# Kernel tuning notes

Measured on AMD Instinct MI355X. Metric: run time of the kernel, lower is better.

Reference implementation:

```python
import jax, jax.numpy as jnp
import numpy as np
import math

B, S, HID = 1, 2048, 4096
HQ, HKV, D = 32, 8, 128
G = HQ // HKV          # GQA group size
OBS, W, SINK = 128, 32, 2
THETA = 500000.0
TOP_FRAC, MID_SPARSITY, LOW_FRAC = 0.05, 0.7, 0.20
K_KEEP = int(math.ceil((1.0 - MID_SPARSITY) * D))  # elements kept per level-1 token


def _rope(x):
    # x: [B, H, S, D]; standard Llama rotary embedding
    half = D // 2
    inv_freq = 1.0 / (THETA ** (jnp.arange(half, dtype=jnp.float32) / half))
    ang = jnp.arange(S, dtype=jnp.float32)[:, None] * inv_freq[None, :]  # [S, half]
    cos = jnp.concatenate([jnp.cos(ang), jnp.cos(ang)], axis=-1)  # [S, D]
    sin = jnp.concatenate([jnp.sin(ang), jnp.sin(ang)], axis=-1)
    x1, x2 = x[..., :half], x[..., half:]
    rot = jnp.concatenate([-x2, x1], axis=-1)
    return x * cos[None, None] + rot * sin[None, None]


def _topk_mask(x):
    # keep the K_KEEP largest-magnitude elements of each length-D token vector
    a = jnp.abs(x)
    thr = jnp.sort(a, axis=-1)[..., D - K_KEEP]
    return a >= thr[..., None]


def setup_inputs() -> dict:
    key = jax.random.key(0)
    ks = jax.random.split(key, 5)
    sc = HID ** -0.5
    return {
        "hidden_states": jax.random.normal(ks[0], (B, S, HID), dtype=jnp.float32),
        "wq": jax.random.normal(ks[1], (HID, HQ * D), dtype=jnp.float32) * sc,
        "wk": jax.random.normal(ks[2], (HID, HKV * D), dtype=jnp.float32) * sc,
        "wv": jax.random.normal(ks[3], (HID, HKV * D), dtype=jnp.float32) * sc,
        "wo": jax.random.normal(ks[4], (HQ * D, HID), dtype=jnp.float32) * sc,
    }


def reference(hidden_states, wq, wk, wv, wo):
    scale = 1.0 / math.sqrt(D)
    q = (hidden_states @ wq).reshape(B, S, HQ, D).transpose(0, 2, 1, 3)   # [B,HQ,S,D]
    k = (hidden_states @ wk).reshape(B, S, HKV, D).transpose(0, 2, 1, 3)  # [B,HKV,S,D]
    v = (hidden_states @ wv).reshape(B, S, HKV, D).transpose(0, 2, 1, 3)
    q, k = _rope(q), _rope(k)

    # --- observation-window GQA attention (grouped queries vs all keys) ---
    obs_q = q[:, :, S - OBS:, :].reshape(B, HKV, G, OBS, D)
    s_obs = jnp.einsum('bhgqd,bhkd->bhgqk', obs_q, k) * scale
    obs_causal = jnp.arange(S)[None, :] <= (S - OBS + jnp.arange(OBS))[:, None]  # [OBS,S]
    s_obs = jnp.where(obs_causal[None, None, None], s_obs, -jnp.inf)
    aw_kv = jax.nn.softmax(s_obs.astype(jnp.float32), axis=-1).mean(axis=2)  # [B,HKV,OBS,S]

    # per-token importance, normalized by how many obs queries observed each key
    counts = jnp.minimum(OBS, S - jnp.arange(S)).astype(jnp.float32)
    imp = aw_kv.sum(axis=2) / counts[None, None, :]  # [B,HKV,S]

    # --- global thresholds over the compressible region -> 3 sparsity levels ---
    imp_c = imp[:, :, :S - W].reshape(-1)
    t_high = jnp.quantile(imp_c, 1.0 - TOP_FRAC)
    t_low = jnp.quantile(imp_c, LOW_FRAC)
    level = jnp.where(imp >= t_high, 0, jnp.where(imp < t_low, 2, 1))
    pos = jnp.arange(S)
    dense_pos = (pos >= S - W) | (pos < SINK)     # recent window + sinks stay dense
    level = jnp.where(dense_pos[None, None, :], 0, level)

    keep_k = jnp.where((level == 0)[..., None], True, (level == 1)[..., None] & _topk_mask(k))
    keep_v = jnp.where((level == 0)[..., None], True, (level == 1)[..., None] & _topk_mask(v))
    k_sp = k * keep_k
    v_sp = v * keep_v
    evicted = level == 2

    # --- causal GQA attention over the sparsified KV cache ---
    q_g = q.reshape(B, HKV, G, S, D)
    s = jnp.einsum('bhgqd,bhkd->bhgqk', q_g, k_sp) * scale
    causal = jnp.tril(jnp.ones((S, S), dtype=bool))
    allow = causal[None, None, None] & (~evicted)[:, :, None, None, :]
    s = jnp.where(allow, s, -jnp.inf)
    p = jax.nn.softmax(s.astype(jnp.float32), axis=-1).astype(v_sp.dtype)
    o = jnp.einsum('bhgqk,bhkd->bhgqd', p, v_sp)
    o = o.reshape(B, HQ, S, D).transpose(0, 2, 1, 3).reshape(B, S, HQ * D)
    return o @ wo
```

## Files before the change

### kernel.cpp

```cpp
#include <hip/hip_runtime.h>
#include <hip/hip_bf16.h>
#include <math.h>

#define S_    2048
#define HID_  4096
#define HQ_   32
#define HKV_  8
#define D_    128
#define G_    4
#define OBS_  128
#define W_    32
#define NKV_  1024
#define NQ_   4096
#define KLD_  2048
#define SCALE_ 0.08838834764831845f
#define THR_IDX_ 89
#define NC_   16128

typedef __attribute__((ext_vector_type(4))) float f32x4;
typedef __attribute__((ext_vector_type(8))) short s16x8;
typedef __attribute__((ext_vector_type(8))) unsigned short u16x8;
typedef __attribute__((ext_vector_type(4))) unsigned short u16x4;
typedef unsigned short ushort_t;

struct TermPtrs { const ushort_t* a[6]; const ushort_t* b[6]; };

__device__ __forceinline__ unsigned short f2bf(float x) {
  union { float f; unsigned u; } v; v.f = x;
  unsigned r = v.u + 0x7FFFu + ((v.u >> 16) & 1u);
  return (unsigned short)(r >> 16);
}
__device__ __forceinline__ float bf2f(unsigned short b) {
  union { unsigned u; float f; } v; v.u = ((unsigned)b) << 16;
  return v.f;
}
__device__ __forceinline__ void gload_lds16(const void* g, void* l) {
  __builtin_amdgcn_global_load_lds((const __attribute__((address_space(1))) unsigned int*)g,
                                   (__attribute__((address_space(3))) unsigned int*)l, 16, 0, 0);
}
__device__ __forceinline__ void term_sel(const TermPtrs& P, int tt,
                                         const ushort_t*& As, const ushort_t*& Bs) {
  switch (tt) {
    case 0: As = P.a[0]; Bs = P.b[0]; break;
    case 1: As = P.a[1]; Bs = P.b[1]; break;
    case 2: As = P.a[2]; Bs = P.b[2]; break;
    case 3: As = P.a[3]; Bs = P.b[3]; break;
    case 4: As = P.a[4]; Bs = P.b[4]; break;
    default: As = P.a[5]; Bs = P.b[5]; break;
  }
}

__global__ __launch_bounds__(256) void split3_kernel(const float* __restrict__ src,
                                                     ushort_t* __restrict__ d0,
                                                     ushort_t* __restrict__ d1,
                                                     ushort_t* __restrict__ d2, int n4) {
  int idx = blockIdx.x * 256 + threadIdx.x;
  if (idx >= n4) return;
  float4 v = ((const float4*)src)[idx];
  u16x4 o0, o1, o2;
  float xs[4] = {v.x, v.y, v.z, v.w};
#pragma unroll
  for (int e = 0; e < 4; ++e) {
    float x = xs[e];
    unsigned short b0 = f2bf(x);
    float r = x - bf2f(b0);
    unsigned short b1 = f2bf(r);
    float r2 = r - bf2f(b1);
    o0[e] = b0; o1[e] = b1; o2[e] = f2bf(r2);
  }
  *(u16x4*)(d0 + (size_t)idx * 4) = o0;
  *(u16x4*)(d1 + (size_t)idx * 4) = o1;
  *(u16x4*)(d2 + (size_t)idx * 4) = o2;
}

__global__ __launch_bounds__(256) void splitT_kernel(const float* __restrict__ src, int N,
                                                     ushort_t* __restrict__ t0,
                                                     ushort_t* __restrict__ t1,
                                                     ushort_t* __restrict__ t2) {
  __shared__ float tile[64][65];
  const int t = threadIdx.x;
  const int n0 = blockIdx.x * 64, k0 = blockIdx.y * 64;
#pragma unroll
  for (int i = 0; i < 16; ++i) {
    int idx = i * 256 + t;
    int r = idx >> 6, c = idx & 63;
    tile[r][c] = src[(size_t)(k0 + r) * N + n0 + c];
  }
  __syncthreads();
#pragma unroll
  for (int i = 0; i < 16; ++i) {
    int idx = i * 256 + t;
    int n = idx >> 6, kk = idx & 63;
    float x = tile[kk][n];
    unsigned short b0 = f2bf(x);
    size_t o = (size_t)(n0 + n) * HID_ + k0 + kk;
    t0[o] = b0;
    if (t1) {
      float r = x - bf2f(b0);
      unsigned short b1 = f2bf(r);
      t1[o] = b1;
      t2[o] = f2bf(r - bf2f(b1));
    }
  }
}

template<int TPZ>
__global__ __launch_bounds__(256) void gemm6(TermPtrs P, float* __restrict__ Cbase,
                                             int M, int N, int K) {
  __shared__ ushort_t lds[2 * 128 * 64];
  const int t = threadIdx.x;
  const int wave = t >> 6, lane = t & 63;
  const int lc = lane & 15, lg = lane >> 4;
  const int bm = blockIdx.y, bn = blockIdx.x, z = blockIdx.z;
  const int wm = wave >> 1, wn = wave & 1;
  const int srow = t >> 3, schunk = t & 7;
  float* C = Cbase + (size_t)z * M * N;

  f32x4 acc[4][4];
#pragma unroll
  for (int fi = 0; fi < 4; ++fi)
#pragma unroll
    for (int fj = 0; fj < 4; ++fj) acc[fi][fj] = 0.f;

  for (int tt = z * TPZ; tt < z * TPZ + TPZ; ++tt) {
    const ushort_t *As, *Bs;
    term_sel(P, tt, As, Bs);
    for (int kb = 0; kb < K / 64; ++kb) {
      __syncthreads();
#pragma unroll
      for (int g = 0; g < 4; ++g) {
        int row = g * 32 + srow;
        int sw = schunk ^ (row & 7);
        gload_lds16(As + (size_t)(bm * 128 + row) * K + kb * 64 + sw * 8,
                    lds + g * 2048 + wave * 512);
        gload_lds16(Bs + (size_t)(bn * 128 + row) * K + kb * 64 + sw * 8,
                    lds + 8192 + g * 2048 + wave * 512);
      }
      __syncthreads();
#pragma unroll
      for (int ks = 0; ks < 2; ++ks) {
        s16x8 af[4], bf[4];
#pragma unroll
        for (int f = 0; f < 4; ++f) {
          int ra = wm * 64 + f * 16 + lc;
          af[f] = *(const s16x8*)(lds + ra * 64 + (((ks * 4 + lg) ^ (ra & 7)) * 8));
          int rb = wn * 64 + f * 16 + lc;
          bf[f] = *(const s16x8*)(lds + 8192 + rb * 64 + (((ks * 4 + lg) ^ (rb & 7)) * 8));
        }
#pragma unroll
        for (int fi = 0; fi < 4; ++fi)
#pragma unroll
          for (int fj = 0; fj < 4; ++fj)
            acc[fi][fj] = __builtin_amdgcn_mfma_f32_16x16x32_bf16(af[fi], bf[fj], acc[fi][fj], 0, 0, 0);
      }
    }
  }
#pragma unroll
  for (int fi = 0; fi < 4; ++fi)
#pragma unroll
    for (int fj = 0; fj < 4; ++fj)
#pragma unroll
      for (int r = 0; r < 4; ++r)
        C[(size_t)(bm * 128 + wm * 64 + fi * 16 + lg * 4 + r) * N +
          bn * 128 + wn * 64 + fj * 16 + lc] = acc[fi][fj][r];
}

__global__ __launch_bounds__(256) void gemm6k(TermPtrs P, float* __restrict__ Cp, int N) {
  __shared__ ushort_t lds[2 * 128 * 64];
  const int t = threadIdx.x;
  const int wave = t >> 6, lane = t & 63;
  const int lc = lane & 15, lg = lane >> 4;
  const int bn = blockIdx.x, z = blockIdx.z;
  const int wm = wave >> 1, wn = wave & 1;
  const int srow = t >> 3, schunk = t & 7;
  float* C = Cp + (size_t)z * 128 * N;

  f32x4 acc[4][4];
#pragma unroll
  for (int fi = 0; fi < 4; ++fi)
#pragma unroll
    for (int fj = 0; fj < 4; ++fj) acc[fi][fj] = 0.f;

  for (int tt = 0; tt < 6; ++tt) {
    const ushort_t *As, *Bs;
    term_sel(P, tt, As, Bs);
    for (int kb = z * 8; kb < z * 8 + 8; ++kb) {
      __syncthreads();
#pragma unroll
      for (int g = 0; g < 4; ++g) {
        int row = g * 32 + srow;
        int sw = schunk ^ (row & 7);
        gload_lds16(As + (size_t)row * HID_ + kb * 64 + sw * 8,
                    lds + g * 2048 + wave * 512);
        gload_lds16(Bs + (size_t)(bn * 128 + row) * HID_ + kb * 64 + sw * 8,
                    lds + 8192 + g * 2048 + wave * 512);
      }
      __syncthreads();
#pragma unroll
      for (int ks = 0; ks < 2; ++ks) {
        s16x8 af[4], bf[4];
#pragma unroll
        for (int f = 0; f < 4; ++f) {
          int ra = wm * 64 + f * 16 + lc;
          af[f] = *(const s16x8*)(lds + ra * 64 + (((ks * 4 + lg) ^ (ra & 7)) * 8));
          int rb = wn * 64 + f * 16 + lc;
          bf[f] = *(const s16x8*)(lds + 8192 + rb * 64 + (((ks * 4 + lg) ^ (rb & 7)) * 8));
        }
#pragma unroll
        for (int fi = 0; fi < 4; ++fi)
#pragma unroll
          for (int fj = 0; fj < 4; ++fj)
            acc[fi][fj] = __builtin_amdgcn_mfma_f32_16x16x32_bf16(af[fi], bf[fj], acc[fi][fj], 0, 0, 0);
      }
    }
  }
#pragma unroll
  for (int fi = 0; fi < 4; ++fi)
#pragma unroll
    for (int fj = 0; fj < 4; ++fj)
#pragma unroll
      for (int r = 0; r < 4; ++r)
        C[(size_t)(wm * 64 + fi * 16 + lg * 4 + r) * N +
          bn * 128 + wn * 64 + fj * 16 + lc] = acc[fi][fj][r];
}

__global__ __launch_bounds__(256) void gemm6z(TermPtrs P, float* __restrict__ Cg) {
  __shared__ ushort_t lds[2 * 128 * 64];
  const int t = threadIdx.x;
  const int wave = t >> 6, lane = t & 63;
  const int lc = lane & 15, lg = lane >> 4;
  const int bm = blockIdx.y, bn = blockIdx.x, z = blockIdx.z;
  const int wm = wave >> 1, wn = wave & 1;
  const int srow = t >> 3, schunk = t & 7;
  const size_t Aoff = (size_t)z * 512 * 128;
  const size_t Boff = (size_t)z * 2048 * 128;
  float* C = Cg + (size_t)z * 512 * 2048;

  f32x4 acc[4][4];
#pragma unroll
  for (int fi = 0; fi < 4; ++fi)
#pragma unroll
    for (int fj = 0; fj < 4; ++fj) acc[fi][fj] = 0.f;

  for (int tt = 0; tt < 6; ++tt) {
    const ushort_t *As, *Bs;
    term_sel(P, tt, As, Bs);
    As += Aoff; Bs += Boff;
    for (int kb = 0; kb < 2; ++kb) {
      __syncthreads();
#pragma unroll
      for (int g = 0; g < 4; ++g) {
        int row = g * 32 + srow;
        int sw = schunk ^ (row & 7);
        gload_lds16(As + (size_t)(bm * 128 + row) * 128 + kb * 64 + sw * 8,
                    lds + g * 2048 + wave * 512);
        gload_lds16(Bs + (size_t)(bn * 128 + row) * 128 + kb * 64 + sw * 8,
                    lds + 8192 + g * 2048 + wave * 512);
      }
      __syncthreads();
#pragma unroll
      for (int ks = 0; ks < 2; ++ks) {
        s16x8 af[4], bf[4];
#pragma unroll
        for (int f = 0; f < 4; ++f) {
          int ra = wm * 64 + f * 16 + lc;
          af[f] = *(const s16x8*)(lds + ra * 64 + (((ks * 4 + lg) ^ (ra & 7)) * 8));
          int rb = wn * 64 + f * 16 + lc;
          bf[f] = *(const s16x8*)(lds + 8192 + rb * 64 + (((ks * 4 + lg) ^ (rb & 7)) * 8));
        }
#pragma unroll
        for (int fi = 0; fi < 4; ++fi)
#pragma unroll
          for (int fj = 0; fj < 4; ++fj)
            acc[fi][fj] = __builtin_amdgcn_mfma_f32_16x16x32_bf16(af[fi], bf[fj], acc[fi][fj], 0, 0, 0);
      }
    }
  }
#pragma unroll
  for (int fi = 0; fi < 4; ++fi)
#pragma unroll
    for (int fj = 0; fj < 4; ++fj)
#pragma unroll
      for (int r = 0; r < 4; ++r)
        C[(size_t)(bm * 128 + wm * 64 + fi * 16 + lg * 4 + r) * 2048 +
          bn * 128 + wn * 64 + fj * 16 + lc] = acc[fi][fj][r];
}

__global__ void reduce3_kernel(const float* __restrict__ p, float* __restrict__ out, int n4) {
  int idx = blockIdx.x * 256 + threadIdx.x;
  if (idx >= n4) return;
  const size_t n = (size_t)n4 * 4;
  float4 a = ((const float4*)p)[idx];
  float4 b = ((const float4*)(p + n))[idx];
  float4 c = ((const float4*)(p + 2 * n))[idx];
  float4 o;
  o.x = a.x + b.x + c.x; o.y = a.y + b.y + c.y;
  o.z = a.z + b.z + c.z; o.w = a.w + b.w + c.w;
  ((float4*)out)[idx] = o;
}
__global__ void reduce8_kernel(const float* __restrict__ Cp, float* __restrict__ out, int n) {
  int idx = blockIdx.x * 256 + threadIdx.x;
  if (idx >= n) return;
  float s = 0.f;
#pragma unroll
  for (int z = 0; z < 8; ++z) s += Cp[(size_t)z * n + idx];
  out[idx] = s;
}

__global__ void freq_kernel(float* __restrict__ invf) {
  int j = threadIdx.x;
  if (j < 64) invf[j] = (float)(1.0 / pow(500000.0, (double)j / 64.0));
}

__global__ void rope_kernel(float* __restrict__ X, ushort_t* __restrict__ Xb,
                            const float* __restrict__ invf, int H, int ld, int pos0, int total) {
  int idx = blockIdx.x * 256 + threadIdx.x;
  if (idx >= total) return;
  int j = idx & 63;
  int h = (idx >> 6) % H;
  int s = idx / (64 * H);
  float ang = (float)(pos0 + s) * invf[j];
  float sn, cs;
  sincosf(ang, &sn, &cs);
  size_t base = (size_t)s * ld + h * D_ + j;
  float x1 = X[base], x2 = X[base + 64];
  float o1 = x1 * cs - x2 * sn;
  float o2 = x2 * cs + x1 * sn;
  X[base] = o1; X[base + 64] = o2;
  if (Xb) { Xb[base] = f2bf(o1); Xb[base + 64] = f2bf(o2); }
}

__global__ __launch_bounds__(256) void splitq_obs(const float* __restrict__ qobs,
                                                  ushort_t* __restrict__ q0,
                                                  ushort_t* __restrict__ q1,
                                                  ushort_t* __restrict__ q2) {
  int idx = blockIdx.x * 256 + threadIdx.x;
  if (idx >= OBS_ * NQ_ / 4) return;
  int idx4 = idx * 4;
  int i = idx4 >> 12;
  int col = idx4 & 4095;
  int hq = col >> 7, d = col & 127;
  int hk = hq >> 2, g = hq & 3;
  float4 v = *(const float4*)(qobs + (size_t)i * NQ_ + col);
  size_t o = (size_t)hk * 65536 + (size_t)(g * 128 + i) * 128 + d;
  float xs[4] = {v.x, v.y, v.z, v.w};
  u16x4 o0, o1, o2;
#pragma unroll
  for (int e = 0; e < 4; ++e) {
    float x = xs[e];
    unsigned short b0 = f2bf(x);
    float r = x - bf2f(b0);
    unsigned short b1 = f2bf(r);
    o0[e] = b0; o1[e] = b1; o2[e] = f2bf(r - bf2f(b1));
  }
  *(u16x4*)(q0 + o) = o0;
  *(u16x4*)(q1 + o) = o1;
  *(u16x4*)(q2 + o) = o2;
}

__global__ __launch_bounds__(256) void splitk_obs(const float* __restrict__ kvf,
                                                  ushort_t* __restrict__ k0,
                                                  ushort_t* __restrict__ k1,
                                                  ushort_t* __restrict__ k2) {
  int idx = blockIdx.x * 256 + threadIdx.x;
  if (idx >= S_ * NKV_ / 4) return;
  int idx4 = idx * 4;
  int j = idx4 >> 10;
  int col = idx4 & 1023;
  int hk = col >> 7, d = col & 127;
  float4 v = *(const float4*)(kvf + (size_t)j * KLD_ + col);
  size_t o = (size_t)hk * 262144 + ((size_t)j << 7) + d;
  float xs[4] = {v.x, v.y, v.z, v.w};
  u16x4 o0, o1, o2;
#pragma unroll
  for (int e = 0; e < 4; ++e) {
    float x = xs[e];
    unsigned short b0 = f2bf(x);
    float r = x - bf2f(b0);
    unsigned short b1 = f2bf(r);
    o0[e] = b0; o1[e] = b1; o2[e] = f2bf(r - bf2f(b1));
  }
  *(u16x4*)(k0 + o) = o0;
  *(u16x4*)(k1 + o) = o1;
  *(u16x4*)(k2 + o) = o2;
}

__global__ __launch_bounds__(256) void rowstat_kernel(const float* __restrict__ s,
                                                      float* __restrict__ mx,
                                                      float* __restrict__ dinv) {
  const int row = blockIdx.x * 4 + (threadIdx.x >> 6);
  const int lane = threadIdx.x & 63;
  const int i = row & 127;
  const int jmax = S_ - OBS_ + i;
  const float* sp = s + (size_t)row * S_;
  float vals[32];
  float m = -INFINITY;
#pragma unroll
  for (int c = 0; c < 8; ++c) {
    int j0 = c * 256 + lane * 4;
    float4 v = *(const float4*)(sp + j0);
    float e0 = (j0 + 0 <= jmax) ? v.x * SCALE_ : -INFINITY;
    float e1 = (j0 + 1 <= jmax) ? v.y * SCALE_ : -INFINITY;
    float e2 = (j0 + 2 <= jmax) ? v.z * SCALE_ : -INFINITY;
    float e3 = (j0 + 3 <= jmax) ? v.w * SCALE_ : -INFINITY;
    vals[c * 4 + 0] = e0; vals[c * 4 + 1] = e1; vals[c * 4 + 2] = e2; vals[c * 4 + 3] = e3;
    m = fmaxf(m, fmaxf(fmaxf(e0, e1), fmaxf(e2, e3)));
  }
#pragma unroll
  for (int off = 1; off < 64; off <<= 1) m = fmaxf(m, __shfl_xor(m, off, 64));
  float ssum = 0.f;
#pragma unroll
  for (int c = 0; c < 32; ++c) ssum += expf(vals[c] - m);
#pragma unroll
  for (int off = 1; off < 64; off <<= 1) ssum += __shfl_xor(ssum, off, 64);
  if (lane == 0) { mx[row] = m; dinv[row] = 1.0f / ssum; }
}

__global__ __launch_bounds__(256) void colsum_part(const float* __restrict__ s,
                                                   const float* __restrict__ mx,
                                                   const float* __restrict__ dinv,
                                                   float* __restrict__ part) {
  __shared__ float mxl[64], dvl[64];
  const int jt = blockIdx.x, hk = blockIdx.y, rc = blockIdx.z;
  const int t = threadIdx.x;
  if (t < 64) {
    mxl[t] = mx[hk * 512 + rc * 64 + t];
    dvl[t] = dinv[hk * 512 + rc * 64 + t];
  }
  __syncthreads();
  const int j = jt * 256 + t;
  const float* sp = s + ((size_t)hk * 512 + rc * 64) * S_ + j;
  float acc = 0.f;
  for (int rr = 0; rr < 64; ++rr) {
    int i = (rc * 64 + rr) & 127;
    if (j <= S_ - OBS_ + i)
      acc += expf(sp[(size_t)rr * S_] * SCALE_ - mxl[rr]) * dvl[rr];
  }
  part[((size_t)rc * 8 + hk) * S_ + j] = acc;
}

__global__ void colsum_fin(const float* __restrict__ part, float* __restrict__ imp) {
  int idx = blockIdx.x * 256 + threadIdx.x;
  int hk = idx >> 11, j = idx & 2047;
  float acc = 0.f;
#pragma unroll
  for (int rc = 0; rc < 8; ++rc) acc += part[((size_t)rc * 8 + hk) * S_ + j];
  float cnt = (float)min(OBS_, S_ - j);
  imp[idx] = acc * 0.25f / cnt;
}

__global__ __launch_bounds__(1024) void radix_all(const float* __restrict__ imp,
                                                  float* __restrict__ thr) {
  __shared__ unsigned hist[4][256];
  __shared__ unsigned pfx_s[4], need_s[4];
  const int t = threadIdx.x;
  if (t < 4) {
    pfx_s[t] = 0u;
    need_s[t] = (t == 0) ? 3225u : (t == 1) ? 3226u : (t == 2) ? 15320u : 15321u;
  }
  __syncthreads();
  for (int pass = 0; pass < 4; ++pass) {
    ((unsigned*)hist)[t] = 0u;
    __syncthreads();
    int shift = 24 - pass * 8;
    for (int idx = t; idx < NC_; idx += 1024) {
      int h = idx / (S_ - W_), j = idx - h * (S_ - W_);
      union { float f; unsigned u; } cv; cv.f = imp[h * S_ + j];
      unsigned u = cv.u;
#pragma unroll
      for (int q = 0; q < 4; ++q) {
        bool m = (pass == 0) || ((u >> (shift + 8)) == (pfx_s[q] >> (shift + 8)));
        if (m) atomicAdd(&hist[q][(u >> shift) & 255u], 1u);
      }
    }
    __syncthreads();
    if (t < 4) {
      unsigned need = need_s[t], cum = 0, pfx = pfx_s[t];
      for (int d = 0; d < 256; ++d) {
        unsigned c = hist[t][d];
        if (cum + c > need) { pfx |= ((unsigned)d) << shift; need_s[t] = need - cum; break; }
        cum += c;
      }
      pfx_s[t] = pfx;
    }
    __syncthreads();
  }
  if (t == 0) {
    union { unsigned u; float f; } c0, c1, c2, c3;
    c0.u = pfx_s[0]; c1.u = pfx_s[1]; c2.u = pfx_s[2]; c3.u = pfx_s[3];
    double fl = 0.2 * (double)(NC_ - 1) - 3225.0;
    double fh = 0.95 * (double)(NC_ - 1) - 15320.0;
    thr[0] = (float)((double)c2.f + ((double)c3.f - (double)c2.f) * fh);
    thr[1] = (float)((double)c0.f + ((double)c1.f - (double)c0.f) * fl);
  }
}

__global__ __launch_bounds__(128) void sparsify_kernel(const float* __restrict__ kv,
                                                       const float* __restrict__ imp,
                                                       const float* __restrict__ thr,
                                                       ushort_t* __restrict__ ksp,
                                                       ushort_t* __restrict__ vsp,
                                                       float* __restrict__ ebias) {
  const int b = blockIdx.x;
  const int j = b >> 3;
  const int h = b & 7;
  const int t = threadIdx.x;
  float ipv = imp[h * S_ + j];
  bool dense = (j >= S_ - W_) || (j < 2);
  int lvl = dense ? 0 : ((ipv >= thr[0]) ? 0 : ((ipv < thr[1]) ? 2 : 1));
  if (t == 0) ebias[h * S_ + j] = (lvl == 2) ? -INFINITY : 0.0f;
  __shared__ float av[128];
  __shared__ float thv;
  size_t base_in = (size_t)j * KLD_ + h * D_;
  size_t base_out = (size_t)j * NKV_ + h * D_;
  float kvv = kv[base_in + t];
  av[t] = fabsf(kvv);
  __syncthreads();
  {
    float at = av[t]; int cnt = 0;
    for (int m = 0; m < 128; ++m) { float am = av[m]; cnt += (am < at) || (am == at && m < t); }
    if (cnt == THR_IDX_) thv = at;
  }
  __syncthreads();
  {
    bool keep = (lvl == 0) || (lvl == 1 && fabsf(kvv) >= thv);
    ksp[base_out + t] = f2bf(keep ? kvv : 0.0f);
  }
  __syncthreads();
  float vvv = kv[base_in + 1024 + t];
  av[t] = fabsf(vvv);
  __syncthreads();
  {
    float at = av[t]; int cnt = 0;
    for (int m = 0; m < 128; ++m) { float am = av[m]; cnt += (am < at) || (am == at && m < t); }
    if (cnt == THR_IDX_) thv = at;
  }
  __syncthreads();
  {
    bool keep = (lvl == 0) || (lvl == 1 && fabsf(vvv) >= thv);
    vsp[base_out + t] = f2bf(keep ? vvv : 0.0f);
  }
}

__global__ __launch_bounds__(256) void vtrans_kernel(const ushort_t* __restrict__ vsp,
                                                     ushort_t* __restrict__ vspT) {
  __shared__ ushort_t tl[64][136];
  const int jt = blockIdx.x;
  const int hk = blockIdx.y;
  const int t = threadIdx.x;
#pragma unroll
  for (int i = 0; i < 4; ++i) {
    int idx = i * 256 + t;
    int j = idx >> 4, c = idx & 15;
    *(u16x8*)&tl[j][c * 8] = *(const u16x8*)(vsp + (size_t)(jt * 64 + j) * NKV_ + hk * 128 + c * 8);
  }
  __syncthreads();
  int d = t >> 1, j0 = (t & 1) * 32;
#pragma unroll
  for (int jj = 0; jj < 4; ++jj) {
    u16x8 v;
#pragma unroll
    for (int e = 0; e < 8; ++e) v[e] = tl[j0 + jj * 8 + e][d];
    *(u16x8*)(vspT + ((size_t)hk * 128 + d) * S_ + jt * 64 + j0 + jj * 8) = v;
  }
}

#define SPAD_ 66
__global__ __launch_bounds__(256) void attn_kernel(const ushort_t* __restrict__ qbp,
                                                   const ushort_t* __restrict__ ksp,
                                                   const ushort_t* __restrict__ vspT,
                                                   const float* __restrict__ ebias,
                                                   ushort_t* __restrict__ ob16) {
  __shared__ ushort_t k_lds[64 * 128];
  __shared__ ushort_t vT_lds[128 * 64];
  __shared__ float s_lds[4][16][SPAD_];
  const int b = blockIdx.x;
  const int xcd = b & 7;
  const int idx = b >> 3;
  const int h = xcd * 4 + (idx >> 4);
  const int p = idx & 15;
  const int hk = h >> 2;
  const int t = threadIdx.x;
  const int w = t >> 6, lane = t & 63;
  const int lc = lane & 15, lg = lane >> 4;

  const ushort_t* kbase = ksp + hk * D_;
  const ushort_t* vbase = vspT + (size_t)hk * D_ * S_;

  for (int strip = 0; strip < 2; ++strip) {
    const int qb = (strip == 0) ? p : 31 - p;
    const int q0 = qb * 64 + w * 16;
    s16x8 qfrag[4];
#pragma unroll
    for (int db = 0; db < 4; ++db)
      qfrag[db] = *(const s16x8*)(qbp + (size_t)(q0 + lc) * NQ_ + h * D_ + db * 32 + lg * 8);

    f32x4 o[8];
#pragma unroll
    for (int n = 0; n < 8; ++n) o[n] = 0.f;
    float mr[4] = {-INFINITY, -INFINITY, -INFINITY, -INFINITY};
    float lr[4] = {0.f, 0.f, 0.f, 0.f};

    const int ntj = qb + 1;
    for (int tj = 0; tj < ntj; ++tj) {
      const int j0 = tj * 64;
      __syncthreads();
#pragma unroll
      for (int i = 0; i < 4; ++i) {
        int slot = i * 256 + w * 64 + lane;
        int row = slot >> 4, c = slot & 15;
        const ushort_t* gp = kbase + (size_t)(j0 + row) * NKV_ + ((c ^ (row & 7)) * 8);
        gload_lds16(gp, &k_lds[(i * 256 + w * 64) * 8]);
      }
#pragma unroll
      for (int i = 0; i < 4; ++i) {
        int slot = i * 256 + w * 64 + lane;
        int d = slot >> 3, c = slot & 7;
        const ushort_t* gp = vbase + (size_t)d * S_ + j0 + ((c ^ (d & 7)) * 8);
        gload_lds16(gp, &vT_lds[(i * 256 + w * 64) * 8]);
      }
      __syncthreads();

      f32x4 sfr[4];
#pragma unroll
      for (int js = 0; js < 4; ++js) sfr[js] = 0.f;
#pragma unroll
      for (int js = 0; js < 4; ++js) {
        int row = js * 16 + lc;
#pragma unroll
        for (int db = 0; db < 4; ++db) {
          s16x8 kf = *(const s16x8*)&k_lds[row * 128 + (((db * 4 + lg) ^ (lc & 7)) * 8)];
          sfr[js] = __builtin_amdgcn_mfma_f32_16x16x32_bf16(qfrag[db], kf, sfr[js], 0, 0, 0);
        }
      }
      float eb[4];
#pragma unroll
      for (int js = 0; js < 4; ++js) eb[js] = ebias[hk * S_ + j0 + js * 16 + lc];

      const bool diag = (tj == qb);
      float sclv[4];
#pragma unroll
      for (int r = 0; r < 4; ++r) {
        float sv[4];
#pragma unroll
        for (int js = 0; js < 4; ++js) sv[js] = sfr[js][r] * SCALE_ + eb[js];
        if (diag) {
          int qrow = w * 16 + lg * 4 + r;
#pragma unroll
          for (int js = 0; js < 4; ++js)
            if (js * 16 + lc > qrow) sv[js] = -INFINITY;
        }
        float tm = fmaxf(fmaxf(sv[0], sv[1]), fmaxf(sv[2], sv[3]));
#pragma unroll
        for (int off = 1; off < 16; off <<= 1) tm = fmaxf(tm, __shfl_xor(tm, off, 64));
        float mnew = fmaxf(mr[r], tm);
        float scl = __expf(mr[r] - mnew);
        float ps = 0.f;
#pragma unroll
        for (int js = 0; js < 4; ++js) {
          float e = __expf(sv[js] - mnew);
          s_lds[w][lg * 4 + r][js * 16 + lc] = e;
          ps += e;
        }
#pragma unroll
        for (int off = 1; off < 16; off <<= 1) ps += __shfl_xor(ps, off, 64);
        lr[r] = lr[r] * scl + ps;
        mr[r] = mnew;
        sclv[r] = scl;
      }
#pragma unroll
      for (int n = 0; n < 8; ++n) {
        f32x4 ov = o[n];
#pragma unroll
        for (int r = 0; r < 4; ++r) ov[r] *= sclv[r];
        o[n] = ov;
      }
      asm volatile("s_waitcnt lgkmcnt(0)" ::: "memory");
      s16x8 pa[2];
#pragma unroll
      for (int ks = 0; ks < 2; ++ks) {
        float pv[8];
        *(f32x4*)&pv[0] = *(const f32x4*)&s_lds[w][lc][ks * 32 + lg * 8];
        *(f32x4*)&pv[4] = *(const f32x4*)&s_lds[w][lc][ks * 32 + lg * 8 + 4];
        s16x8 pk;
#pragma unroll
        for (int e = 0; e < 8; ++e) pk[e] = (short)f2bf(pv[e]);
        pa[ks] = pk;
      }
#pragma unroll
      for (int n = 0; n < 8; ++n) {
        int d = n * 16 + lc;
#pragma unroll
        for (int ks = 0; ks < 2; ++ks) {
          s16x8 vf = *(const s16x8*)&vT_lds[d * 64 + (((ks * 4 + lg) ^ (lc & 7)) * 8)];
          o[n] = __builtin_amdgcn_mfma_f32_16x16x32_bf16(pa[ks], vf, o[n], 0, 0, 0);
        }
      }
    }
#pragma unroll
    for (int r = 0; r < 4; ++r) {
      float rinv = 1.0f / lr[r];
      int row = q0 + lg * 4 + r;
#pragma unroll
      for (int n = 0; n < 8; ++n)
        ob16[(size_t)row * NQ_ + h * D_ + n * 16 + lc] = f2bf(o[n][r] * rinv);
    }
  }
}

extern "C" void kernel_launch(void* const* d_in, const int* in_sizes, int n_in,
                              void* d_out, int out_size, void* d_ws, size_t ws_size,
                              hipStream_t stream) {
  (void)in_sizes; (void)n_in; (void)out_size; (void)ws_size;
  const float* hid = (const float*)d_in[0];
  const float* wq  = (const float*)d_in[1];
  const float* wk  = (const float*)d_in[2];
  const float* wv  = (const float*)d_in[3];
  const float* wo  = (const float*)d_in[4];
  float* out = (float*)d_out;
  char* ws = (char*)d_ws;
  const size_t MB = 1ull << 20;

  ushort_t* h0     = (ushort_t*)(ws + 0 * MB);
  ushort_t* h1     = (ushort_t*)(ws + 16 * MB);
  ushort_t* h2     = (ushort_t*)(ws + 32 * MB);
  ushort_t* wq0T   = (ushort_t*)(ws + 48 * MB);
  ushort_t* wq1T   = (ushort_t*)(ws + 80 * MB);
  ushort_t* wq2T   = (ushort_t*)(ws + 112 * MB);
  ushort_t* wkv0T  = (ushort_t*)(ws + 144 * MB);
  ushort_t* wkv1T  = (ushort_t*)(ws + 160 * MB);
  ushort_t* wkv2T  = (ushort_t*)(ws + 176 * MB);
  float*    qpart  = (float*)(ws + 192 * MB);
  float*    qobs   = (float*)(ws + 208 * MB);
  float*    kvf    = (float*)(ws + 210 * MB);
  float*    kvp    = (float*)(ws + 80 * MB);
  float*    qf     = (float*)(ws + 80 * MB);
  ushort_t* qb16   = (ushort_t*)(ws + 112 * MB);
  float*    s_obs  = (float*)(ws + 0 * MB);
  ushort_t* woT    = (ushort_t*)(ws + 144 * MB);
  ushort_t* ksp    = (ushort_t*)(ws + 176 * MB);
  ushort_t* vsp    = (ushort_t*)(ws + 180 * MB);
  ushort_t* vspT   = (ushort_t*)(ws + 184 * MB);
  ushort_t* ob16   = (ushort_t*)(ws + 188 * MB);
  ushort_t* qo0    = (ushort_t*)(ws + 32 * MB);
  ushort_t* qo1    = (ushort_t*)(ws + 33 * MB);
  ushort_t* qo2    = (ushort_t*)(ws + 34 * MB);
  ushort_t* kb0    = (ushort_t*)(ws + 35 * MB);
  ushort_t* kb1    = (ushort_t*)(ws + 39 * MB);
  ushort_t* kb2    = (ushort_t*)(ws + 43 * MB);
  char*     misc   = ws + 226 * MB;
  float*    impv   = (float*)(misc + 0);
  float*    eb     = (float*)(misc + 64 * 1024);
  float*    invf   = (float*)(misc + 128 * 1024);
  float*    thr    = (float*)(misc + 132 * 1024);
  float*    mxbuf  = (float*)(misc + 160 * 1024);
  float*    dinvb  = (float*)(misc + 192 * 1024);
  float*    part   = (float*)(misc + 256 * 1024);

  split3_kernel<<<(S_ * HID_ / 4 + 255) / 256, 256, 0, stream>>>(hid, h0, h1, h2, S_ * HID_ / 4);
  splitT_kernel<<<dim3(NQ_ / 64, HID_ / 64), 256, 0, stream>>>(wq, NQ_, wq0T, wq1T, wq2T);
  splitT_kernel<<<dim3(NKV_ / 64, HID_ / 64), 256, 0, stream>>>(wk, NKV_, wkv0T, wkv1T, wkv2T);
  splitT_kernel<<<dim3(NKV_ / 64, HID_ / 64), 256, 0, stream>>>(
      wv, NKV_, wkv0T + (size_t)NKV_ * HID_, wkv1T + (size_t)NKV_ * HID_, wkv2T + (size_t)NKV_ * HID_);

  const size_t obs_off = (size_t)(S_ - OBS_) * HID_;
  {
    TermPtrs P;
    P.a[0] = h0 + obs_off; P.b[0] = wq0T;
    P.a[1] = h0 + obs_off; P.b[1] = wq1T;
    P.a[2] = h1 + obs_off; P.b[2] = wq0T;
    P.a[3] = h1 + obs_off; P.b[3] = wq1T;
    P.a[4] = h0 + obs_off; P.b[4] = wq2T;
    P.a[5] = h2 + obs_off; P.b[5] = wq0T;
    gemm6k<<<dim3(NQ_ / 128, 1, 8), 256, 0, stream>>>(P, qpart, NQ_);
  }
  reduce8_kernel<<<(OBS_ * NQ_ + 255) / 256, 256, 0, stream>>>(qpart, qobs, OBS_ * NQ_);

  {
    TermPtrs P;
    P.a[0] = h0; P.b[0] = wkv0T;
    P.a[1] = h0; P.b[1] = wkv1T;
    P.a[2] = h1; P.b[2] = wkv0T;
    P.a[3] = h1; P.b[3] = wkv1T;
    P.a[4] = h0; P.b[4] = wkv2T;
    P.a[5] = h2; P.b[5] = wkv0T;
    gemm6<2><<<dim3(KLD_ / 128, S_ / 128, 3), 256, 0, stream>>>(P, kvp, S_, KLD_, HID_);
  }
  reduce3_kernel<<<(S_ * KLD_ / 4 + 255) / 256, 256, 0, stream>>>(kvp, kvf, S_ * KLD_ / 4);

  {
    TermPtrs P;
    for (int i = 0; i < 6; ++i) { P.a[i] = h0; P.b[i] = wq0T; }
    gemm6<1><<<dim3(NQ_ / 128, S_ / 128, 1), 256, 0, stream>>>(P, qf, S_, NQ_, HID_);
  }

  splitT_kernel<<<dim3(HID_ / 64, HID_ / 64), 256, 0, stream>>>(wo, HID_, woT, nullptr, nullptr);

  freq_kernel<<<1, 64, 0, stream>>>(invf);
  rope_kernel<<<(S_ * HQ_ * 64 + 255) / 256, 256, 0, stream>>>(qf, qb16, invf, HQ_, NQ_, 0, S_ * HQ_ * 64);
  rope_kernel<<<(S_ * HKV_ * 64 + 255) / 256, 256, 0, stream>>>(kvf, nullptr, invf, HKV_, KLD_, 0, S_ * HKV_ * 64);
  rope_kernel<<<(OBS_ * HQ_ * 64 + 255) / 256, 256, 0, stream>>>(qobs, nullptr, invf, HQ_, NQ_, S_ - OBS_, OBS_ * HQ_ * 64);

  splitq_obs<<<(OBS_ * NQ_ / 4 + 255) / 256, 256, 0, stream>>>(qobs, qo0, qo1, qo2);
  splitk_obs<<<(S_ * NKV_ / 4 + 255) / 256, 256, 0, stream>>>(kvf, kb0, kb1, kb2);
  {
    TermPtrs P;
    P.a[0] = qo0; P.b[0] = kb0;
    P.a[1] = qo0; P.b[1] = kb1;
    P.a[2] = qo1; P.b[2] = kb0;
    P.a[3] = qo1; P.b[3] = kb1;
    P.a[4] = qo0; P.b[4] = kb2;
    P.a[5] = qo2; P.b[5] = kb0;
    gemm6z<<<dim3(16, 4, 8), 256, 0, stream>>>(P, s_obs);
  }
  rowstat_kernel<<<1024, 256, 0, stream>>>(s_obs, mxbuf, dinvb);
  colsum_part<<<dim3(8, 8, 8), 256, 0, stream>>>(s_obs, mxbuf, dinvb, part);
  colsum_fin<<<64, 256, 0, stream>>>(part, impv);

  radix_all<<<1, 1024, 0, stream>>>(impv, thr);

  sparsify_kernel<<<S_ * HKV_, 128, 0, stream>>>(kvf, impv, thr, ksp, vsp, eb);
  vtrans_kernel<<<dim3(S_ / 64, HKV_), 256, 0, stream>>>(vsp, vspT);
  attn_kernel<<<512, 256, 0, stream>>>(qb16, ksp, vspT, eb, ob16);
  {
    TermPtrs P;
    for (int i = 0; i < 6; ++i) { P.a[i] = ob16; P.b[i] = woT; }
    gemm6<1><<<dim3(HID_ / 128, S_ / 128, 1), 256, 0, stream>>>(P, out, S_, HID_, HID_);
  }
}
```

Measured before the change: 973.7 us.

## Share operand tiles in KV split GEMM, split-K Q/O GEMMs, fuse RoPE with splits

The KV projection GEMM now loads one shared operand tile plus two partner tiles per z-slice, so each LDS stage feeds two MFMAs and redundant global loads of the shared operand are avoided. The full-Q and output projection GEMMs use a two-way split-K to raise block count, with the partial sums folded into the RoPE kernel or a small reduce. Separate reduce, RoPE and bf16-split kernels for the observation queries and keys are merged into single passes. In exchange, LDS use rises, the split-K path adds extra partial-buffer traffic and a reduction, and the workspace buffer offsets are reshuffled.

```diff
diff --git a/kernel.cpp b/kernel.cpp
--- a/kernel.cpp
+++ b/kernel.cpp
@@ -24,6 +24,7 @@
 typedef unsigned short ushort_t;
 
 struct TermPtrs { const ushort_t* a[6]; const ushort_t* b[6]; };
+struct KvSh { const ushort_t* S[3]; const ushort_t* U0[3]; const ushort_t* U1[3]; int ash[3]; };
 
 __device__ __forceinline__ unsigned short f2bf(float x) {
   union { float f; unsigned u; } v; v.f = x;
@@ -65,8 +66,7 @@
     unsigned short b0 = f2bf(x);
     float r = x - bf2f(b0);
     unsigned short b1 = f2bf(r);
-    float r2 = r - bf2f(b1);
-    o0[e] = b0; o1[e] = b1; o2[e] = f2bf(r2);
+    o0[e] = b0; o1[e] = b1; o2[e] = f2bf(r - bf2f(b1));
   }
   *(u16x4*)(d0 + (size_t)idx * 4) = o0;
   *(u16x4*)(d1 + (size_t)idx * 4) = o1;
@@ -104,9 +104,86 @@
   }
 }
 
-template<int TPZ>
-__global__ __launch_bounds__(256) void gemm6(TermPtrs P, float* __restrict__ Cbase,
-                                             int M, int N, int K) {
+__global__ __launch_bounds__(256) void gemm_kvsh(KvSh P, float* __restrict__ Cbase,
+                                                 int M, int N, int K) {
+  __shared__ ushort_t lds[3 * 128 * 64];
+  const int t = threadIdx.x;
+  const int wave = t >> 6, lane = t & 63;
+  const int lc = lane & 15, lg = lane >> 4;
+  const int bm = blockIdx.y, bn = blockIdx.x, z = blockIdx.z;
+  const int wm = wave >> 1, wn = wave & 1;
+  const int srow = t >> 3, schunk = t & 7;
+  const int ash = P.ash[z];
+  const ushort_t* Sp  = P.S[z];
+  const ushort_t* U0p = P.U0[z];
+  const ushort_t* U1p = P.U1[z];
+  float* C = Cbase + (size_t)z * M * N;
+  const int sbase = (ash ? bm : bn) * 128;
+  const int ubase = (ash ? bn : bm) * 128;
+
+  f32x4 acc[4][4];
+#pragma unroll
+  for (int fi = 0; fi < 4; ++fi)
+#pragma unroll
+    for (int fj = 0; fj < 4; ++fj) acc[fi][fj] = 0.f;
+
+  for (int kb = 0; kb < K / 64; ++kb) {
+    __syncthreads();
+#pragma unroll
+    for (int g = 0; g < 4; ++g) {
+      int row = g * 32 + srow;
+      int sw = schunk ^ (row & 7);
+      size_t co = kb * 64 + sw * 8;
+      gload_lds16(Sp  + (size_t)(sbase + row) * K + co, lds + g * 2048 + wave * 512);
+      gload_lds16(U0p + (size_t)(ubase + row) * K + co, lds + 8192 + g * 2048 + wave * 512);
+      gload_lds16(U1p + (size_t)(ubase + row) * K + co, lds + 16384 + g * 2048 + wave * 512);
+    }
+    __syncthreads();
+#pragma unroll
+    for (int ks = 0; ks < 2; ++ks) {
+      s16x8 sf[4], u0f[4], u1f[4];
+#pragma unroll
+      for (int f = 0; f < 4; ++f) {
+        int rs = (ash ? wm : wn) * 64 + f * 16 + lc;
+        sf[f] = *(const s16x8*)(lds + rs * 64 + (((ks * 4 + lg) ^ (rs & 7)) * 8));
+        int ru = (ash ? wn : wm) * 64 + f * 16 + lc;
+        int cu = (((ks * 4 + lg) ^ (ru & 7)) * 8);
+        u0f[f] = *(const s16x8*)(lds + 8192 + ru * 64 + cu);
+        u1f[f] = *(const s16x8*)(lds + 16384 + ru * 64 + cu);
+      }
+      if (ash) {
+#pragma unroll
+        for (int fi = 0; fi < 4; ++fi)
+#pragma unroll
+          for (int fj = 0; fj < 4; ++fj) {
+            acc[fi][fj] = __builtin_amdgcn_mfma_f32_16x16x32_bf16(sf[fi], u0f[fj], acc[fi][fj], 0, 0, 0);
+            acc[fi][fj] = __builtin_amdgcn_mfma_f32_16x16x32_bf16(sf[fi], u1f[fj], acc[fi][fj], 0, 0, 0);
+          }
+      } else {
+#pragma unroll
+        for (int fi = 0; fi < 4; ++fi)
+#pragma unroll
+          for (int fj = 0; fj < 4; ++fj) {
+            acc[fi][fj] = __builtin_amdgcn_mfma_f32_16x16x32_bf16(u0f[fi], sf[fj], acc[fi][fj], 0, 0, 0);
+            acc[fi][fj] = __builtin_amdgcn_mfma_f32_16x16x32_bf16(u1f[fi], sf[fj], acc[fi][fj], 0, 0, 0);
+          }
+      }
+    }
+  }
+#pragma unroll
+  for (int fi = 0; fi < 4; ++fi)
+#pragma unroll
+    for (int fj = 0; fj < 4; ++fj)
+#pragma unroll
+      for (int r = 0; r < 4; ++r)
+        C[(size_t)(bm * 128 + wm * 64 + fi * 16 + lg * 4 + r) * N +
+          bn * 128 + wn * 64 + fj * 16 + lc] = acc[fi][fj][r];
+}
+
+__global__ __launch_bounds__(256) void gemm1(const ushort_t* __restrict__ A,
+                                             const ushort_t* __restrict__ B,
+                                             float* __restrict__ Cbase,
+                                             int M, int N, int K, int KSTEPS) {
   __shared__ ushort_t lds[2 * 128 * 64];
   const int t = threadIdx.x;
   const int wave = t >> 6, lane = t & 63;
@@ -122,37 +199,32 @@
 #pragma unroll
     for (int fj = 0; fj < 4; ++fj) acc[fi][fj] = 0.f;
 
-  for (int tt = z * TPZ; tt < z * TPZ + TPZ; ++tt) {
-    const ushort_t *As, *Bs;
-    term_sel(P, tt, As, Bs);
-    for (int kb = 0; kb < K / 64; ++kb) {
-      __syncthreads();
-#pragma unroll
-      for (int g = 0; g < 4; ++g) {
-        int row = g * 32 + srow;
-        int sw = schunk ^ (row & 7);
-        gload_lds16(As + (size_t)(bm * 128 + row) * K + kb * 64 + sw * 8,
-                    lds + g * 2048 + wave * 512);
-        gload_lds16(Bs + (size_t)(bn * 128 + row) * K + kb * 64 + sw * 8,
-                    lds + 8192 + g * 2048 + wave * 512);
-      }
-      __syncthreads();
-#pragma unroll
-      for (int ks = 0; ks < 2; ++ks) {
-        s16x8 af[4], bf[4];
-#pragma unroll
-        for (int f = 0; f < 4; ++f) {
-          int ra = wm * 64 + f * 16 + lc;
-          af[f] = *(const s16x8*)(lds + ra * 64 + (((ks * 4 + lg) ^ (ra & 7)) * 8));
-          int rb = wn * 64 + f * 16 + lc;
-          bf[f] = *(const s16x8*)(lds + 8192 + rb * 64 + (((ks * 4 + lg) ^ (rb & 7)) * 8));
-        }
-#pragma unroll
-        for (int fi = 0; fi < 4; ++fi)
-#pragma unroll
-          for (int fj = 0; fj < 4; ++fj)
-            acc[fi][fj] = __builtin_amdgcn_mfma_f32_16x16x32_bf16(af[fi], bf[fj], acc[fi][fj], 0, 0, 0);
-      }
+  for (int kb = z * KSTEPS; kb < z * KSTEPS + KSTEPS; ++kb) {
+    __syncthreads();
+#pragma unroll
+    for (int g = 0; g < 4; ++g) {
+      int row = g * 32 + srow;
+      int sw = schunk ^ (row & 7);
+      size_t co = kb * 64 + sw * 8;
+      gload_lds16(A + (size_t)(bm * 128 + row) * K + co, lds + g * 2048 + wave * 512);
+      gload_lds16(B + (size_t)(bn * 128 + row) * K + co, lds + 8192 + g * 2048 + wave * 512);
+    }
+    __syncthreads();
+#pragma unroll
+    for (int ks = 0; ks < 2; ++ks) {
+      s16x8 af[4], bf[4];
+#pragma unroll
+      for (int f = 0; f < 4; ++f) {
+        int ra = wm * 64 + f * 16 + lc;
+        af[f] = *(const s16x8*)(lds + ra * 64 + (((ks * 4 + lg) ^ (ra & 7)) * 8));
+        int rb = wn * 64 + f * 16 + lc;
+        bf[f] = *(const s16x8*)(lds + 8192 + rb * 64 + (((ks * 4 + lg) ^ (rb & 7)) * 8));
+      }
+#pragma unroll
+      for (int fi = 0; fi < 4; ++fi)
+#pragma unroll
+        for (int fj = 0; fj < 4; ++fj)
+          acc[fi][fj] = __builtin_amdgcn_mfma_f32_16x16x32_bf16(af[fi], bf[fj], acc[fi][fj], 0, 0, 0);
     }
   }
 #pragma unroll
@@ -298,13 +370,15 @@
   o.z = a.z + b.z + c.z; o.w = a.w + b.w + c.w;
   ((float4*)out)[idx] = o;
 }
-__global__ void reduce8_kernel(const float* __restrict__ Cp, float* __restrict__ out, int n) {
+__global__ void reduce2_kernel(const float* __restrict__ p, float* __restrict__ out, int n4) {
   int idx = blockIdx.x * 256 + threadIdx.x;
-  if (idx >= n) return;
-  float s = 0.f;
-#pragma unroll
-  for (int z = 0; z < 8; ++z) s += Cp[(size_t)z * n + idx];
-  out[idx] = s;
+  if (idx >= n4) return;
+  const size_t n = (size_t)n4 * 4;
+  float4 a = ((const float4*)p)[idx];
+  float4 b = ((const float4*)(p + n))[idx];
+  float4 o;
+  o.x = a.x + b.x; o.y = a.y + b.y; o.z = a.z + b.z; o.w = a.w + b.w;
+  ((float4*)out)[idx] = o;
 }
 
 __global__ void freq_kernel(float* __restrict__ invf) {
@@ -312,77 +386,82 @@
   if (j < 64) invf[j] = (float)(1.0 / pow(500000.0, (double)j / 64.0));
 }
 
-__global__ void rope_kernel(float* __restrict__ X, ushort_t* __restrict__ Xb,
-                            const float* __restrict__ invf, int H, int ld, int pos0, int total) {
+__global__ __launch_bounds__(256) void qobs_fuse(const float* __restrict__ qpart,
+                                                 const float* __restrict__ invf,
+                                                 ushort_t* __restrict__ q0,
+                                                 ushort_t* __restrict__ q1,
+                                                 ushort_t* __restrict__ q2) {
   int idx = blockIdx.x * 256 + threadIdx.x;
-  if (idx >= total) return;
   int j = idx & 63;
-  int h = (idx >> 6) % H;
-  int s = idx / (64 * H);
-  float ang = (float)(pos0 + s) * invf[j];
-  float sn, cs;
-  sincosf(ang, &sn, &cs);
-  size_t base = (size_t)s * ld + h * D_ + j;
-  float x1 = X[base], x2 = X[base + 64];
+  int hq = (idx >> 6) & 31;
+  int i = idx >> 11;
+  size_t base = (size_t)i * NQ_ + hq * 128 + j;
+  float x1 = 0.f, x2 = 0.f;
+#pragma unroll
+  for (int z = 0; z < 8; ++z) {
+    x1 += qpart[(size_t)z * OBS_ * NQ_ + base];
+    x2 += qpart[(size_t)z * OBS_ * NQ_ + base + 64];
+  }
+  float ang = (float)(S_ - OBS_ + i) * invf[j];
+  float sn, cs; sincosf(ang, &sn, &cs);
   float o1 = x1 * cs - x2 * sn;
   float o2 = x2 * cs + x1 * sn;
-  X[base] = o1; X[base + 64] = o2;
-  if (Xb) { Xb[base] = f2bf(o1); Xb[base + 64] = f2bf(o2); }
-}
-
-__global__ __launch_bounds__(256) void splitq_obs(const float* __restrict__ qobs,
-                                                  ushort_t* __restrict__ q0,
-                                                  ushort_t* __restrict__ q1,
-                                                  ushort_t* __restrict__ q2) {
-  int idx = blockIdx.x * 256 + threadIdx.x;
-  if (idx >= OBS_ * NQ_ / 4) return;
-  int idx4 = idx * 4;
-  int i = idx4 >> 12;
-  int col = idx4 & 4095;
-  int hq = col >> 7, d = col & 127;
   int hk = hq >> 2, g = hq & 3;
-  float4 v = *(const float4*)(qobs + (size_t)i * NQ_ + col);
-  size_t o = (size_t)hk * 65536 + (size_t)(g * 128 + i) * 128 + d;
-  float xs[4] = {v.x, v.y, v.z, v.w};
-  u16x4 o0, o1, o2;
-#pragma unroll
-  for (int e = 0; e < 4; ++e) {
-    float x = xs[e];
+  size_t o = (size_t)hk * 65536 + (size_t)(g * 128 + i) * 128 + j;
+  float ys[2] = {o1, o2};
+#pragma unroll
+  for (int e = 0; e < 2; ++e) {
+    float x = ys[e];
     unsigned short b0 = f2bf(x);
     float r = x - bf2f(b0);
     unsigned short b1 = f2bf(r);
-    o0[e] = b0; o1[e] = b1; o2[e] = f2bf(r - bf2f(b1));
-  }
-  *(u16x4*)(q0 + o) = o0;
-  *(u16x4*)(q1 + o) = o1;
-  *(u16x4*)(q2 + o) = o2;
-}
-
-__global__ __launch_bounds__(256) void splitk_obs(const float* __restrict__ kvf,
-                                                  ushort_t* __restrict__ k0,
-                                                  ushort_t* __restrict__ k1,
-                                                  ushort_t* __restrict__ k2) {
+    q0[o + e * 64] = b0; q1[o + e * 64] = b1; q2[o + e * 64] = f2bf(r - bf2f(b1));
+  }
+}
+
+__global__ __launch_bounds__(256) void ropekv_splitk(float* __restrict__ kvf,
+                                                     const float* __restrict__ invf,
+                                                     ushort_t* __restrict__ k0,
+                                                     ushort_t* __restrict__ k1,
+                                                     ushort_t* __restrict__ k2) {
   int idx = blockIdx.x * 256 + threadIdx.x;
-  if (idx >= S_ * NKV_ / 4) return;
-  int idx4 = idx * 4;
-  int j = idx4 >> 10;
-  int col = idx4 & 1023;
-  int hk = col >> 7, d = col & 127;
-  float4 v = *(const float4*)(kvf + (size_t)j * KLD_ + col);
-  size_t o = (size_t)hk * 262144 + ((size_t)j << 7) + d;
-  float xs[4] = {v.x, v.y, v.z, v.w};
-  u16x4 o0, o1, o2;
-#pragma unroll
-  for (int e = 0; e < 4; ++e) {
-    float x = xs[e];
+  int j = idx & 63;
+  int h = (idx >> 6) & 7;
+  int s = idx >> 9;
+  size_t base = (size_t)s * KLD_ + h * 128 + j;
+  float x1 = kvf[base], x2 = kvf[base + 64];
+  float ang = (float)s * invf[j];
+  float sn, cs; sincosf(ang, &sn, &cs);
+  float o1 = x1 * cs - x2 * sn;
+  float o2 = x2 * cs + x1 * sn;
+  kvf[base] = o1; kvf[base + 64] = o2;
+  size_t o = (size_t)h * 262144 + (size_t)s * 128 + j;
+  float ys[2] = {o1, o2};
+#pragma unroll
+  for (int e = 0; e < 2; ++e) {
+    float x = ys[e];
     unsigned short b0 = f2bf(x);
     float r = x - bf2f(b0);
     unsigned short b1 = f2bf(r);
-    o0[e] = b0; o1[e] = b1; o2[e] = f2bf(r - bf2f(b1));
-  }
-  *(u16x4*)(k0 + o) = o0;
-  *(u16x4*)(k1 + o) = o1;
-  *(u16x4*)(k2 + o) = o2;
+    k0[o + e * 64] = b0; k1[o + e * 64] = b1; k2[o + e * 64] = f2bf(r - bf2f(b1));
+  }
+}
+
+__global__ __launch_bounds__(256) void rope_q_fuse(const float* __restrict__ qp,
+                                                   const float* __restrict__ invf,
+                                                   ushort_t* __restrict__ qb16) {
+  int idx = blockIdx.x * 256 + threadIdx.x;
+  int j = idx & 63;
+  int h = (idx >> 6) & 31;
+  int s = idx >> 11;
+  size_t base = (size_t)s * NQ_ + h * 128 + j;
+  const size_t zs = (size_t)S_ * NQ_;
+  float x1 = qp[base] + qp[base + zs];
+  float x2 = qp[base + 64] + qp[base + 64 + zs];
+  float ang = (float)s * invf[j];
+  float sn, cs; sincosf(ang, &sn, &cs);
+  qb16[base] = f2bf(x1 * cs - x2 * sn);
+  qb16[base + 64] = f2bf(x2 * cs + x1 * sn);
 }
 
 __global__ __launch_bounds__(256) void rowstat_kernel(const float* __restrict__ s,
@@ -731,24 +810,24 @@
   ushort_t* wkv1T  = (ushort_t*)(ws + 160 * MB);
   ushort_t* wkv2T  = (ushort_t*)(ws + 176 * MB);
   float*    qpart  = (float*)(ws + 192 * MB);
-  float*    qobs   = (float*)(ws + 208 * MB);
-  float*    kvf    = (float*)(ws + 210 * MB);
+  float*    kvf    = (float*)(ws + 192 * MB);
   float*    kvp    = (float*)(ws + 80 * MB);
-  float*    qf     = (float*)(ws + 80 * MB);
-  ushort_t* qb16   = (ushort_t*)(ws + 112 * MB);
-  float*    s_obs  = (float*)(ws + 0 * MB);
+  float*    qp2    = (float*)(ws + 80 * MB);
+  ushort_t* qb16   = (ushort_t*)(ws + 16 * MB);
+  ushort_t* kb0    = (ushort_t*)(ws + 32 * MB);
+  ushort_t* kb1    = (ushort_t*)(ws + 36 * MB);
+  ushort_t* kb2    = (ushort_t*)(ws + 40 * MB);
+  float*    s_obs  = (float*)(ws + 48 * MB);
   ushort_t* woT    = (ushort_t*)(ws + 144 * MB);
   ushort_t* ksp    = (ushort_t*)(ws + 176 * MB);
   ushort_t* vsp    = (ushort_t*)(ws + 180 * MB);
   ushort_t* vspT   = (ushort_t*)(ws + 184 * MB);
-  ushort_t* ob16   = (ushort_t*)(ws + 188 * MB);
-  ushort_t* qo0    = (ushort_t*)(ws + 32 * MB);
-  ushort_t* qo1    = (ushort_t*)(ws + 33 * MB);
-  ushort_t* qo2    = (ushort_t*)(ws + 34 * MB);
-  ushort_t* kb0    = (ushort_t*)(ws + 35 * MB);
-  ushort_t* kb1    = (ushort_t*)(ws + 39 * MB);
-  ushort_t* kb2    = (ushort_t*)(ws + 43 * MB);
-  char*     misc   = ws + 226 * MB;
+  ushort_t* ob16   = (ushort_t*)(ws + 188 * MB + 512 * 1024);
+  float*    opart  = (float*)(ws + 0 * MB);
+  ushort_t* qo0    = (ushort_t*)(ws + 208 * MB);
+  ushort_t* qo1    = (ushort_t*)(ws + 209 * MB);
+  ushort_t* qo2    = (ushort_t*)(ws + 210 * MB);
+  char*     misc   = ws + 212 * MB;
   float*    impv   = (float*)(misc + 0);
   float*    eb     = (float*)(misc + 64 * 1024);
   float*    invf   = (float*)(misc + 128 * 1024);
@@ -756,6 +835,8 @@
   float*    mxbuf  = (float*)(misc + 160 * 1024);
   float*    dinvb  = (float*)(misc + 192 * 1024);
   float*    part   = (float*)(misc + 256 * 1024);
+
+  freq_kernel<<<1, 64, 0, stream>>>(invf);
 
   split3_kernel<<<(S_ * HID_ / 4 + 255) / 256, 256, 0, stream>>>(hid, h0, h1, h2, S_ * HID_ / 4);
   splitT_kernel<<<dim3(NQ_ / 64, HID_ / 64), 256, 0, stream>>>(wq, NQ_, wq0T, wq1T, wq2T);
@@ -774,35 +855,24 @@
     P.a[5] = h2 + obs_off; P.b[5] = wq0T;
     gemm6k<<<dim3(NQ_ / 128, 1, 8), 256, 0, stream>>>(P, qpart, NQ_);
   }
-  reduce8_kernel<<<(OBS_ * NQ_ + 255) / 256, 256, 0, stream>>>(qpart, qobs, OBS_ * NQ_);
+  qobs_fuse<<<(OBS_ * HQ_ * 64) / 256, 256, 0, stream>>>(qpart, invf, qo0, qo1, qo2);
 
   {
-    TermPtrs P;
-    P.a[0] = h0; P.b[0] = wkv0T;
-    P.a[1] = h0; P.b[1] = wkv1T;
-    P.a[2] = h1; P.b[2] = wkv0T;
-    P.a[3] = h1; P.b[3] = wkv1T;
-    P.a[4] = h0; P.b[4] = wkv2T;
-    P.a[5] = h2; P.b[5] = wkv0T;
-    gemm6<2><<<dim3(KLD_ / 128, S_ / 128, 3), 256, 0, stream>>>(P, kvp, S_, KLD_, HID_);
+    KvSh P;
+    P.S[0] = h0;    P.U0[0] = wkv1T; P.U1[0] = wkv2T; P.ash[0] = 1;
+    P.S[1] = h1;    P.U0[1] = wkv0T; P.U1[1] = wkv1T; P.ash[1] = 1;
+    P.S[2] = wkv0T; P.U0[2] = h0;    P.U1[2] = h2;    P.ash[2] = 0;
+    gemm_kvsh<<<dim3(KLD_ / 128, S_ / 128, 3), 256, 0, stream>>>(P, kvp, S_, KLD_, HID_);
   }
   reduce3_kernel<<<(S_ * KLD_ / 4 + 255) / 256, 256, 0, stream>>>(kvp, kvf, S_ * KLD_ / 4);
 
-  {
-    TermPtrs P;
-    for (int i = 0; i < 6; ++i) { P.a[i] = h0; P.b[i] = wq0T; }
-    gemm6<1><<<dim3(NQ_ / 128, S_ / 128, 1), 256, 0, stream>>>(P, qf, S_, NQ_, HID_);
-  }
+  gemm1<<<dim3(NQ_ / 128, S_ / 128, 2), 256, 0, stream>>>(h0, wq0T, qp2, S_, NQ_, HID_, 32);
 
   splitT_kernel<<<dim3(HID_ / 64, HID_ / 64), 256, 0, stream>>>(wo, HID_, woT, nullptr, nullptr);
 
-  freq_kernel<<<1, 64, 0, stream>>>(invf);
-  rope_kernel<<<(S_ * HQ_ * 64 + 255) / 256, 256, 0, stream>>>(qf, qb16, invf, HQ_, NQ_, 0, S_ * HQ_ * 64);
-  rope_kernel<<<(S_ * HKV_ * 64 + 255) / 256, 256, 0, stream>>>(kvf, nullptr, invf, HKV_, KLD_, 0, S_ * HKV_ * 64);
-  rope_kernel<<<(OBS_ * HQ_ * 64 + 255) / 256, 256, 0, stream>>>(qobs, nullptr, invf, HQ_, NQ_, S_ - OBS_, OBS_ * HQ_ * 64);
-
-  splitq_obs<<<(OBS_ * NQ_ / 4 + 255) / 256, 256, 0, stream>>>(qobs, qo0, qo1, qo2);
-  splitk_obs<<<(S_ * NKV_ / 4 + 255) / 256, 256, 0, stream>>>(kvf, kb0, kb1, kb2);
+  rope_q_fuse<<<(S_ * HQ_ * 64) / 256, 256, 0, stream>>>(qp2, invf, qb16);
+  ropekv_splitk<<<(S_ * HKV_ * 64) / 256, 256, 0, stream>>>(kvf, invf, kb0, kb1, kb2);
+
   {
     TermPtrs P;
     P.a[0] = qo0; P.b[0] = kb0;
@@ -822,9 +892,6 @@
   sparsify_kernel<<<S_ * HKV_, 128, 0, stream>>>(kvf, impv, thr, ksp, vsp, eb);
   vtrans_kernel<<<dim3(S_ / 64, HKV_), 256, 0, stream>>>(vsp, vspT);
   attn_kernel<<<512, 256, 0, stream>>>(qb16, ksp, vspT, eb, ob16);
-  {
-    TermPtrs P;
-    for (int i = 0; i < 6; ++i) { P.a[i] = ob16; P.b[i] = woT; }
-    gemm6<1><<<dim3(HID_ / 128, S_ / 128, 1), 256, 0, stream>>>(P, out, S_, HID_, HID_);
-  }
-}
+  gemm1<<<dim3(HID_ / 128, S_ / 128, 2), 256, 0, stream>>>(ob16, woT, opart, S_, HID_, HID_, 32);
+  reduce2_kernel<<<(S_ * HID_ / 4 + 255) / 256, 256, 0, stream>>>(opart, out, S_ * HID_ / 4);
+}
```

New measurement: 1.049 ms. +7.7%, slower.
